# Optimization experiments

Hardware: AMD Instinct MI355X
Metric: run time of the kernel (lower is better)

Reference implementation:

```python
import jax, jax.numpy as jnp
import numpy as np

H, F, E, K = 1024, 4096, 8, 2
B, S = 2, 2048

def setup_inputs() -> dict:
    key = jax.random.key(0)
    ks = jax.random.split(key, 5)
    scale = 0.02
    return {
        "x": jax.random.normal(ks[0], (B, S, H), dtype=jnp.float32),
        "router_w": jax.random.normal(ks[1], (H, E), dtype=jnp.float32) * scale,
        "router_b": jnp.zeros((E,), dtype=jnp.float32),
        "w1": jax.random.normal(ks[2], (E, H, F), dtype=jnp.float32) * scale,
        "b1": jnp.zeros((E, F), dtype=jnp.float32),
        "w2": jax.random.normal(ks[3], (E, F, H), dtype=jnp.float32) * scale,
        "b2": jnp.zeros((E, H), dtype=jnp.float32),
        "k": K,
    }

def reference(x, router_w, router_b, w1, b1, w2, b2, k):
    # Router: softmax over experts, then top-k
    scores = jnp.einsum('bsh,he->bse', x, router_w) + router_b          # [B,S,E]
    probs = jax.nn.softmax(scores, axis=-1)
    p, expert_id = jax.lax.top_k(probs, k)                               # [B,S,k]
    # Dense all-expert MLP (math identical to per-expert gather/scatter)
    h = jax.nn.gelu(jnp.einsum('bsh,ehf->bsef', x, w1) + b1,
                    approximate=False)                                    # [B,S,E,F]
    out_all = jnp.einsum('bsef,efh->bseh', h, w2) + b2                    # [B,S,E,H]
    # Gather the k selected experts per token
    out = jnp.take_along_axis(out_all, expert_id[..., None], axis=2)     # [B,S,k,H]
    # Normalize top-k probs and combine
    p = p / jnp.sum(p, axis=-1, keepdims=True)                            # [B,S,k]
    return jnp.sum(p[..., None] * out, axis=2)                            # [B,S,H]
```

## Files before the change

### kernel.cpp

```cpp
#include <hip/hip_runtime.h>
#include <hip/hip_bf16.h>
#include <math.h>

#define H 1024
#define F 4096
#define E 8
#define NTOK 4096
#define CAP 4096
#define MCAP 2048
#define NPAIR 8192

typedef unsigned short u16;
typedef __bf16 bf16x8 __attribute__((ext_vector_type(8)));
typedef float f32x4 __attribute__((ext_vector_type(4)));
typedef u16 u16x8 __attribute__((ext_vector_type(8)));

__device__ inline u16 f2bf(float f) {
    union { float f; unsigned u; } v; v.f = f;
    unsigned r = v.u + 0x7fffu + ((v.u >> 16) & 1u);
    return (u16)(r >> 16);
}

__global__ void cvt_x(const float* __restrict__ x, u16* __restrict__ xb, int n4) {
    int j = blockIdx.x * blockDim.x + threadIdx.x;
    if (j >= n4) return;
    float4 v = ((const float4*)x)[j];
    u16x8 dummy; (void)dummy;
    u16* o = xb + (size_t)j * 4;
    o[0] = f2bf(v.x); o[1] = f2bf(v.y); o[2] = f2bf(v.z); o[3] = f2bf(v.w);
}

__global__ void transpose_cvt(const float* __restrict__ in, u16* __restrict__ out,
                              int R, int C) {
    const float* ip = in + (size_t)blockIdx.z * R * C;
    u16* op = out + (size_t)blockIdx.z * R * C;
    __shared__ float tile[32][33];
    int c0 = blockIdx.x * 32, r0 = blockIdx.y * 32;
    int tx = threadIdx.x, ty = threadIdx.y;
    for (int j = ty; j < 32; j += 8)
        tile[j][tx] = ip[(size_t)(r0 + j) * C + c0 + tx];
    __syncthreads();
    for (int j = ty; j < 32; j += 8)
        op[(size_t)(c0 + j) * R + r0 + tx] = f2bf(tile[tx][j]);
}

__global__ void router_kernel(const float* __restrict__ x, const float* __restrict__ rw,
                              const float* __restrict__ rb, int* __restrict__ counts,
                              int* __restrict__ tok_e, float* __restrict__ wgt_e) {
    int tok = blockIdx.x;
    int lane = threadIdx.x;
    float s[E] = {0.f,0.f,0.f,0.f,0.f,0.f,0.f,0.f};
    for (int r = 0; r < 4; ++r) {
        int h = r * 256 + lane * 4;
        float4 xv = *(const float4*)&x[(size_t)tok * H + h];
        const float* xf = (const float*)&xv;
        #pragma unroll
        for (int u = 0; u < 4; ++u) {
            float xs = xf[u];
            const float4* row = (const float4*)&rw[(size_t)(h + u) * E];
            float4 a = row[0], b = row[1];
            s[0] += xs * a.x; s[1] += xs * a.y; s[2] += xs * a.z; s[3] += xs * a.w;
            s[4] += xs * b.x; s[5] += xs * b.y; s[6] += xs * b.z; s[7] += xs * b.w;
        }
    }
    #pragma unroll
    for (int off = 32; off > 0; off >>= 1)
        #pragma unroll
        for (int e2 = 0; e2 < E; ++e2) s[e2] += __shfl_down(s[e2], off);
    if (lane == 0) {
        #pragma unroll
        for (int e2 = 0; e2 < E; ++e2) s[e2] += rb[e2];
        int i0 = 0;
        #pragma unroll
        for (int e2 = 1; e2 < E; ++e2) if (s[e2] > s[i0]) i0 = e2;
        int i1 = (i0 == 0) ? 1 : 0;
        #pragma unroll
        for (int e2 = 0; e2 < E; ++e2) if (e2 != i0 && s[e2] > s[i1]) i1 = e2;
        float p0 = 1.0f / (1.0f + expf(s[i1] - s[i0]));
        float p1 = 1.0f - p0;
        int pos0 = atomicAdd(&counts[i0], 1);
        tok_e[i0 * CAP + pos0] = tok; wgt_e[i0 * CAP + pos0] = p0;
        int pos1 = atomicAdd(&counts[i1], 1);
        tok_e[i1 * CAP + pos1] = tok; wgt_e[i1 * CAP + pos1] = p1;
    }
}

__global__ void scan_kernel(const int* __restrict__ counts, int* __restrict__ offsets) {
    if (threadIdx.x == 0 && blockIdx.x == 0) {
        int acc = 0;
        for (int e2 = 0; e2 < E; ++e2) { offsets[e2] = acc; acc += counts[e2]; }
    }
}

#define BM 128
#define BN 128
#define BK 32
#define LDP 40

__global__ void gemm1_kernel(const u16* __restrict__ xb, const u16* __restrict__ w1t,
                             const float* __restrict__ b1,
                             const int* __restrict__ counts, const int* __restrict__ offsets,
                             const int* __restrict__ tok_e, u16* __restrict__ hbuf) {
    int e = blockIdx.z;
    int rows = counts[e];
    int m0 = blockIdx.y * BM;
    if (m0 >= rows) return;
    int n0 = blockIdx.x * BN;
    int off = offsets[e];
    const u16* wB = w1t + (size_t)e * F * H;

    __shared__ u16 As[BM][LDP];
    __shared__ u16 Bs[BN][LDP];

    int tid = threadIdx.x;
    int lane = tid & 63;
    int w = tid >> 6;
    int wr = w >> 1, wc = w & 1;

    int ar0 = tid >> 2, ac0 = tid & 3;
    int ar1 = ar0 + 64;
    int ia0 = m0 + ar0; if (ia0 > rows - 1) ia0 = rows - 1;
    int ia1 = m0 + ar1; if (ia1 > rows - 1) ia1 = rows - 1;
    int t0 = tok_e[e * CAP + ia0];
    int t1 = tok_e[e * CAP + ia1];
    const u16* aR0 = xb + (size_t)t0 * H + ac0 * 8;
    const u16* aR1 = xb + (size_t)t1 * H + ac0 * 8;
    const u16* bR0 = wB + (size_t)(n0 + ar0) * H + ac0 * 8;
    const u16* bR1 = wB + (size_t)(n0 + ar1) * H + ac0 * 8;

    f32x4 acc[4][4] = {};

    for (int k0 = 0; k0 < H; k0 += BK) {
        u16x8 av0 = *(const u16x8*)(aR0 + k0);
        u16x8 av1 = *(const u16x8*)(aR1 + k0);
        u16x8 bv0 = *(const u16x8*)(bR0 + k0);
        u16x8 bv1 = *(const u16x8*)(bR1 + k0);
        __syncthreads();
        *(u16x8*)&As[ar0][ac0 * 8] = av0;
        *(u16x8*)&As[ar1][ac0 * 8] = av1;
        *(u16x8*)&Bs[ar0][ac0 * 8] = bv0;
        *(u16x8*)&Bs[ar1][ac0 * 8] = bv1;
        __syncthreads();
        bf16x8 af[4], bfr[4];
        int fr = lane & 15, fk = (lane >> 4) * 8;
        #pragma unroll
        for (int m = 0; m < 4; ++m) af[m] = *(bf16x8*)&As[wr * 64 + m * 16 + fr][fk];
        #pragma unroll
        for (int n = 0; n < 4; ++n) bfr[n] = *(bf16x8*)&Bs[wc * 64 + n * 16 + fr][fk];
        #pragma unroll
        for (int m = 0; m < 4; ++m)
            #pragma unroll
            for (int n = 0; n < 4; ++n)
                acc[m][n] = __builtin_amdgcn_mfma_f32_16x16x32_bf16(af[m], bfr[n], acc[m][n], 0, 0, 0);
    }

    const float* b1e = b1 + (size_t)e * F;
    int cr = (lane >> 4) * 4;
    int cc = lane & 15;
    #pragma unroll
    for (int m = 0; m < 4; ++m) {
        int gr = m0 + wr * 64 + m * 16 + cr;
        #pragma unroll
        for (int n = 0; n < 4; ++n) {
            int gc = n0 + wc * 64 + n * 16 + cc;
            float bias = b1e[gc];
            #pragma unroll
            for (int j = 0; j < 4; ++j) {
                int r = gr + j;
                if (r < rows) {
                    float v = acc[m][n][j] + bias;
                    float g = 0.5f * v * (1.0f + erff(v * 0.70710678118654752f));
                    hbuf[(size_t)(off + r) * F + gc] = f2bf(g);
                }
            }
        }
    }
}

__global__ void gemm2_kernel(const u16* __restrict__ hbuf, const u16* __restrict__ w2t,
                             const float* __restrict__ b2,
                             const int* __restrict__ counts, const int* __restrict__ offsets,
                             const int* __restrict__ tok_e, const float* __restrict__ wgt_e,
                             float* __restrict__ out) {
    int e = blockIdx.z;
    int rows = counts[e];
    int m0 = blockIdx.y * BM;
    if (m0 >= rows) return;
    int n0 = blockIdx.x * BN;
    int off = offsets[e];
    const u16* wB = w2t + (size_t)e * H * F;

    __shared__ u16 As[BM][LDP];
    __shared__ u16 Bs[BN][LDP];

    int tid = threadIdx.x;
    int lane = tid & 63;
    int w = tid >> 6;
    int wr = w >> 1, wc = w & 1;

    int ar0 = tid >> 2, ac0 = tid & 3;
    int ar1 = ar0 + 64;
    int ia0 = m0 + ar0; if (ia0 > rows - 1) ia0 = rows - 1;
    int ia1 = m0 + ar1; if (ia1 > rows - 1) ia1 = rows - 1;
    const u16* aR0 = hbuf + (size_t)(off + ia0) * F + ac0 * 8;
    const u16* aR1 = hbuf + (size_t)(off + ia1) * F + ac0 * 8;
    const u16* bR0 = wB + (size_t)(n0 + ar0) * F + ac0 * 8;
    const u16* bR1 = wB + (size_t)(n0 + ar1) * F + ac0 * 8;

    f32x4 acc[4][4] = {};

    for (int k0 = 0; k0 < F; k0 += BK) {
        u16x8 av0 = *(const u16x8*)(aR0 + k0);
        u16x8 av1 = *(const u16x8*)(aR1 + k0);
        u16x8 bv0 = *(const u16x8*)(bR0 + k0);
        u16x8 bv1 = *(const u16x8*)(bR1 + k0);
        __syncthreads();
        *(u16x8*)&As[ar0][ac0 * 8] = av0;
        *(u16x8*)&As[ar1][ac0 * 8] = av1;
        *(u16x8*)&Bs[ar0][ac0 * 8] = bv0;
        *(u16x8*)&Bs[ar1][ac0 * 8] = bv1;
        __syncthreads();
        bf16x8 af[4], bfr[4];
        int fr = lane & 15, fk = (lane >> 4) * 8;
        #pragma unroll
        for (int m = 0; m < 4; ++m) af[m] = *(bf16x8*)&As[wr * 64 + m * 16 + fr][fk];
        #pragma unroll
        for (int n = 0; n < 4; ++n) bfr[n] = *(bf16x8*)&Bs[wc * 64 + n * 16 + fr][fk];
        #pragma unroll
        for (int m = 0; m < 4; ++m)
            #pragma unroll
            for (int n = 0; n < 4; ++n)
                acc[m][n] = __builtin_amdgcn_mfma_f32_16x16x32_bf16(af[m], bfr[n], acc[m][n], 0, 0, 0);
    }

    const float* b2e = b2 + (size_t)e * H;
    int cr = (lane >> 4) * 4;
    int cc = lane & 15;
    #pragma unroll
    for (int m = 0; m < 4; ++m) {
        int gr = m0 + wr * 64 + m * 16 + cr;
        #pragma unroll
        for (int j = 0; j < 4; ++j) {
            int r = gr + j;
            if (r < rows) {
                int tok = tok_e[e * CAP + r];
                float wgt = wgt_e[e * CAP + r];
                #pragma unroll
                for (int n = 0; n < 4; ++n) {
                    int gc = n0 + wc * 64 + n * 16 + cc;
                    float v = (acc[m][n][j] + b2e[gc]) * wgt;
                    atomicAdd(&out[(size_t)tok * H + gc], v);
                }
            }
        }
    }
}

extern "C" void kernel_launch(void* const* d_in, const int* in_sizes, int n_in,
                              void* d_out, int out_size, void* d_ws, size_t ws_size,
                              hipStream_t stream) {
    const float* x  = (const float*)d_in[0];
    const float* rw = (const float*)d_in[1];
    const float* rb = (const float*)d_in[2];
    const float* w1 = (const float*)d_in[3];
    const float* b1 = (const float*)d_in[4];
    const float* w2 = (const float*)d_in[5];
    const float* b2 = (const float*)d_in[6];
    float* out = (float*)d_out;

    char* ws = (char*)d_ws;
    size_t o = 0;
    u16* xb   = (u16*)(ws + o); o += (size_t)NTOK * H * 2;
    u16* w1t  = (u16*)(ws + o); o += (size_t)E * F * H * 2;
    u16* w2t  = (u16*)(ws + o); o += (size_t)E * H * F * 2;
    u16* hbuf = (u16*)(ws + o); o += (size_t)NPAIR * F * 2;
    int*   tok_e = (int*)(ws + o);   o += (size_t)E * CAP * 4;
    float* wgt_e = (float*)(ws + o); o += (size_t)E * CAP * 4;
    int*   counts  = (int*)(ws + o); o += E * 4;
    int*   offsets = (int*)(ws + o); o += E * 4;

    hipMemsetAsync(counts, 0, 2 * E * sizeof(int), stream);
    hipMemsetAsync(out, 0, (size_t)out_size * sizeof(float), stream);

    cvt_x<<<(NTOK * H / 4 + 255) / 256, 256, 0, stream>>>(x, xb, NTOK * H / 4);
    transpose_cvt<<<dim3(F / 32, H / 32, E), dim3(32, 8), 0, stream>>>(w1, w1t, H, F);
    transpose_cvt<<<dim3(H / 32, F / 32, E), dim3(32, 8), 0, stream>>>(w2, w2t, F, H);
    router_kernel<<<NTOK, 64, 0, stream>>>(x, rw, rb, counts, tok_e, wgt_e);
    scan_kernel<<<1, 64, 0, stream>>>(counts, offsets);
    gemm1_kernel<<<dim3(F / BN, MCAP / BM, E), 256, 0, stream>>>(xb, w1t, b1, counts, offsets, tok_e, hbuf);
    gemm2_kernel<<<dim3(H / BN, MCAP / BM, E), 256, 0, stream>>>(hbuf, w2t, b2, counts, offsets, tok_e, wgt_e, out);
}
```

Before: 800.5 us.

## Use direct global-to-LDS loads in expert GEMMs and vectorize conversion kernels

The expert GEMMs now stage tiles with global_load_lds (buffer loads that write straight into LDS), dropping the register round trip and padded LDS layout. MFMA operands are swapped so each lane holds four consecutive columns, which allows vector bias loads and 8-byte bf16 stores in the GELU epilogue. The x-conversion and weight transpose kernels use wider vector loads and stores with 64x64 tiles. The grid M dimension grows from MCAP to CAP to cover experts with more than 2048 tokens, which fixes a correctness risk but launches more early-exit blocks. The unpadded LDS layout may cause bank conflicts on fragment reads.

Result: faster. 776.2 us (-3.0%).

```diff
diff --git a/kernel.cpp b/kernel.cpp
--- a/kernel.cpp
+++ b/kernel.cpp
@@ -7,13 +7,13 @@
 #define E 8
 #define NTOK 4096
 #define CAP 4096
-#define MCAP 2048
 #define NPAIR 8192
 
 typedef unsigned short u16;
 typedef __bf16 bf16x8 __attribute__((ext_vector_type(8)));
 typedef float f32x4 __attribute__((ext_vector_type(4)));
 typedef u16 u16x8 __attribute__((ext_vector_type(8)));
+typedef u16 u16x4 __attribute__((ext_vector_type(4)));
 
 __device__ inline u16 f2bf(float f) {
     union { float f; unsigned u; } v; v.f = f;
@@ -21,27 +21,50 @@
     return (u16)(r >> 16);
 }
 
-__global__ void cvt_x(const float* __restrict__ x, u16* __restrict__ xb, int n4) {
+__device__ inline void gload_lds16(const void* g, void* l) {
+    __builtin_amdgcn_global_load_lds(
+        (const __attribute__((address_space(1))) unsigned*)g,
+        (__attribute__((address_space(3))) unsigned*)l, 16, 0, 0);
+}
+
+__global__ void cvt_x(const float* __restrict__ x, u16* __restrict__ xb, int n8) {
     int j = blockIdx.x * blockDim.x + threadIdx.x;
-    if (j >= n4) return;
-    float4 v = ((const float4*)x)[j];
-    u16x8 dummy; (void)dummy;
-    u16* o = xb + (size_t)j * 4;
-    o[0] = f2bf(v.x); o[1] = f2bf(v.y); o[2] = f2bf(v.z); o[3] = f2bf(v.w);
+    if (j >= n8) return;
+    const float4* p = (const float4*)(x + (size_t)j * 8);
+    float4 a = p[0], b = p[1];
+    u16x8 o;
+    o[0] = f2bf(a.x); o[1] = f2bf(a.y); o[2] = f2bf(a.z); o[3] = f2bf(a.w);
+    o[4] = f2bf(b.x); o[5] = f2bf(b.y); o[6] = f2bf(b.z); o[7] = f2bf(b.w);
+    *(u16x8*)(xb + (size_t)j * 8) = o;
 }
 
 __global__ void transpose_cvt(const float* __restrict__ in, u16* __restrict__ out,
                               int R, int C) {
     const float* ip = in + (size_t)blockIdx.z * R * C;
     u16* op = out + (size_t)blockIdx.z * R * C;
-    __shared__ float tile[32][33];
-    int c0 = blockIdx.x * 32, r0 = blockIdx.y * 32;
-    int tx = threadIdx.x, ty = threadIdx.y;
-    for (int j = ty; j < 32; j += 8)
-        tile[j][tx] = ip[(size_t)(r0 + j) * C + c0 + tx];
+    __shared__ float tile[64][65];
+    int r0 = blockIdx.y * 64, c0 = blockIdx.x * 64;
+    int tid = threadIdx.x;
+    int rr = tid >> 4;
+    int cc4 = (tid & 15) * 4;
+    #pragma unroll
+    for (int it = 0; it < 4; ++it) {
+        int r = rr + it * 16;
+        float4 v = *(const float4*)&ip[(size_t)(r0 + r) * C + c0 + cc4];
+        tile[r][cc4 + 0] = v.x; tile[r][cc4 + 1] = v.y;
+        tile[r][cc4 + 2] = v.z; tile[r][cc4 + 3] = v.w;
+    }
     __syncthreads();
-    for (int j = ty; j < 32; j += 8)
-        op[(size_t)(c0 + j) * R + r0 + tx] = f2bf(tile[tx][j]);
+    int co = tid >> 3;
+    int ro8 = (tid & 7) * 8;
+    #pragma unroll
+    for (int it = 0; it < 2; ++it) {
+        int c = co + it * 32;
+        u16x8 o;
+        #pragma unroll
+        for (int u = 0; u < 8; ++u) o[u] = f2bf(tile[ro8 + u][c]);
+        *(u16x8*)&op[(size_t)(c0 + c) * R + r0 + ro8] = o;
+    }
 }
 
 __global__ void router_kernel(const float* __restrict__ x, const float* __restrict__ rw,
@@ -95,7 +118,6 @@
 #define BM 128
 #define BN 128
 #define BK 32
-#define LDP 40
 
 __global__ void gemm1_kernel(const u16* __restrict__ xb, const u16* __restrict__ w1t,
                              const float* __restrict__ b1,
@@ -109,69 +131,69 @@
     int off = offsets[e];
     const u16* wB = w1t + (size_t)e * F * H;
 
-    __shared__ u16 As[BM][LDP];
-    __shared__ u16 Bs[BN][LDP];
-
-    int tid = threadIdx.x;
-    int lane = tid & 63;
-    int w = tid >> 6;
+    __shared__ u16 As[BM * BK];
+    __shared__ u16 Bs[BN * BK];
+
+    int tid = threadIdx.x, lane = tid & 63, w = tid >> 6;
     int wr = w >> 1, wc = w & 1;
 
-    int ar0 = tid >> 2, ac0 = tid & 3;
-    int ar1 = ar0 + 64;
-    int ia0 = m0 + ar0; if (ia0 > rows - 1) ia0 = rows - 1;
-    int ia1 = m0 + ar1; if (ia1 > rows - 1) ia1 = rows - 1;
-    int t0 = tok_e[e * CAP + ia0];
-    int t1 = tok_e[e * CAP + ia1];
-    const u16* aR0 = xb + (size_t)t0 * H + ac0 * 8;
-    const u16* aR1 = xb + (size_t)t1 * H + ac0 * 8;
-    const u16* bR0 = wB + (size_t)(n0 + ar0) * H + ac0 * 8;
-    const u16* bR1 = wB + (size_t)(n0 + ar1) * H + ac0 * 8;
+    int i0 = w * 2, i1 = w * 2 + 1;
+    int rA0 = i0 * 16 + (lane >> 2), rA1 = i1 * 16 + (lane >> 2);
+    int cB = (lane & 3) * 8;
+    int ia0 = m0 + rA0; if (ia0 >= rows) ia0 = rows - 1;
+    int ia1 = m0 + rA1; if (ia1 >= rows) ia1 = rows - 1;
+    const u16* aS0 = xb + (size_t)tok_e[e * CAP + ia0] * H + cB;
+    const u16* aS1 = xb + (size_t)tok_e[e * CAP + ia1] * H + cB;
+    const u16* bS0 = wB + (size_t)(n0 + rA0) * H + cB;
+    const u16* bS1 = wB + (size_t)(n0 + rA1) * H + cB;
+    u16* lA0 = As + i0 * 512;  u16* lA1 = As + i1 * 512;
+    u16* lB0 = Bs + i0 * 512;  u16* lB1 = Bs + i1 * 512;
+
+    int fr = lane & 15, fk = (lane >> 4) * 8;
+    const u16* pa = As + (wr * 64 + fr) * BK + fk;
+    const u16* pb = Bs + (wc * 64 + fr) * BK + fk;
 
     f32x4 acc[4][4] = {};
 
     for (int k0 = 0; k0 < H; k0 += BK) {
-        u16x8 av0 = *(const u16x8*)(aR0 + k0);
-        u16x8 av1 = *(const u16x8*)(aR1 + k0);
-        u16x8 bv0 = *(const u16x8*)(bR0 + k0);
-        u16x8 bv1 = *(const u16x8*)(bR1 + k0);
         __syncthreads();
-        *(u16x8*)&As[ar0][ac0 * 8] = av0;
-        *(u16x8*)&As[ar1][ac0 * 8] = av1;
-        *(u16x8*)&Bs[ar0][ac0 * 8] = bv0;
-        *(u16x8*)&Bs[ar1][ac0 * 8] = bv1;
+        gload_lds16(aS0 + k0, lA0);
+        gload_lds16(aS1 + k0, lA1);
+        gload_lds16(bS0 + k0, lB0);
+        gload_lds16(bS1 + k0, lB1);
         __syncthreads();
         bf16x8 af[4], bfr[4];
-        int fr = lane & 15, fk = (lane >> 4) * 8;
-        #pragma unroll
-        for (int m = 0; m < 4; ++m) af[m] = *(bf16x8*)&As[wr * 64 + m * 16 + fr][fk];
-        #pragma unroll
-        for (int n = 0; n < 4; ++n) bfr[n] = *(bf16x8*)&Bs[wc * 64 + n * 16 + fr][fk];
+        #pragma unroll
+        for (int m = 0; m < 4; ++m) af[m] = *(const bf16x8*)(pa + m * 16 * BK);
+        #pragma unroll
+        for (int n = 0; n < 4; ++n) bfr[n] = *(const bf16x8*)(pb + n * 16 * BK);
         #pragma unroll
         for (int m = 0; m < 4; ++m)
             #pragma unroll
             for (int n = 0; n < 4; ++n)
-                acc[m][n] = __builtin_amdgcn_mfma_f32_16x16x32_bf16(af[m], bfr[n], acc[m][n], 0, 0, 0);
+                acc[m][n] = __builtin_amdgcn_mfma_f32_16x16x32_bf16(bfr[n], af[m], acc[m][n], 0, 0, 0);
     }
 
     const float* b1e = b1 + (size_t)e * F;
-    int cr = (lane >> 4) * 4;
-    int cc = lane & 15;
+    int c4 = (lane >> 4) * 4;
     #pragma unroll
     for (int m = 0; m < 4; ++m) {
-        int gr = m0 + wr * 64 + m * 16 + cr;
-        #pragma unroll
-        for (int n = 0; n < 4; ++n) {
-            int gc = n0 + wc * 64 + n * 16 + cc;
-            float bias = b1e[gc];
+        int r = m0 + wr * 64 + m * 16 + fr;
+        if (r < rows) {
+            u16* hrow = hbuf + (size_t)(off + r) * F;
             #pragma unroll
-            for (int j = 0; j < 4; ++j) {
-                int r = gr + j;
-                if (r < rows) {
-                    float v = acc[m][n][j] + bias;
+            for (int n = 0; n < 4; ++n) {
+                int gc = n0 + wc * 64 + n * 16 + c4;
+                float4 bv = *(const float4*)&b1e[gc];
+                const float* bvf = (const float*)&bv;
+                u16x4 ov;
+                #pragma unroll
+                for (int j = 0; j < 4; ++j) {
+                    float v = acc[m][n][j] + bvf[j];
                     float g = 0.5f * v * (1.0f + erff(v * 0.70710678118654752f));
-                    hbuf[(size_t)(off + r) * F + gc] = f2bf(g);
+                    ov[j] = f2bf(g);
                 }
+                *(u16x4*)&hrow[gc] = ov;
             }
         }
     }
@@ -190,67 +212,66 @@
     int off = offsets[e];
     const u16* wB = w2t + (size_t)e * H * F;
 
-    __shared__ u16 As[BM][LDP];
-    __shared__ u16 Bs[BN][LDP];
-
-    int tid = threadIdx.x;
-    int lane = tid & 63;
-    int w = tid >> 6;
+    __shared__ u16 As[BM * BK];
+    __shared__ u16 Bs[BN * BK];
+
+    int tid = threadIdx.x, lane = tid & 63, w = tid >> 6;
     int wr = w >> 1, wc = w & 1;
 
-    int ar0 = tid >> 2, ac0 = tid & 3;
-    int ar1 = ar0 + 64;
-    int ia0 = m0 + ar0; if (ia0 > rows - 1) ia0 = rows - 1;
-    int ia1 = m0 + ar1; if (ia1 > rows - 1) ia1 = rows - 1;
-    const u16* aR0 = hbuf + (size_t)(off + ia0) * F + ac0 * 8;
-    const u16* aR1 = hbuf + (size_t)(off + ia1) * F + ac0 * 8;
-    const u16* bR0 = wB + (size_t)(n0 + ar0) * F + ac0 * 8;
-    const u16* bR1 = wB + (size_t)(n0 + ar1) * F + ac0 * 8;
+    int i0 = w * 2, i1 = w * 2 + 1;
+    int rA0 = i0 * 16 + (lane >> 2), rA1 = i1 * 16 + (lane >> 2);
+    int cB = (lane & 3) * 8;
+    int ia0 = m0 + rA0; if (ia0 >= rows) ia0 = rows - 1;
+    int ia1 = m0 + rA1; if (ia1 >= rows) ia1 = rows - 1;
+    const u16* aS0 = hbuf + (size_t)(off + ia0) * F + cB;
+    const u16* aS1 = hbuf + (size_t)(off + ia1) * F + cB;
+    const u16* bS0 = wB + (size_t)(n0 + rA0) * F + cB;
+    const u16* bS1 = wB + (size_t)(n0 + rA1) * F + cB;
+    u16* lA0 = As + i0 * 512;  u16* lA1 = As + i1 * 512;
+    u16* lB0 = Bs + i0 * 512;  u16* lB1 = Bs + i1 * 512;
+
+    int fr = lane & 15, fk = (lane >> 4) * 8;
+    const u16* pa = As + (wr * 64 + fr) * BK + fk;
+    const u16* pb = Bs + (wc * 64 + fr) * BK + fk;
 
     f32x4 acc[4][4] = {};
 
     for (int k0 = 0; k0 < F; k0 += BK) {
-        u16x8 av0 = *(const u16x8*)(aR0 + k0);
-        u16x8 av1 = *(const u16x8*)(aR1 + k0);
-        u16x8 bv0 = *(const u16x8*)(bR0 + k0);
-        u16x8 bv1 = *(const u16x8*)(bR1 + k0);
         __syncthreads();
-        *(u16x8*)&As[ar0][ac0 * 8] = av0;
-        *(u16x8*)&As[ar1][ac0 * 8] = av1;
-        *(u16x8*)&Bs[ar0][ac0 * 8] = bv0;
-        *(u16x8*)&Bs[ar1][ac0 * 8] = bv1;
+        gload_lds16(aS0 + k0, lA0);
+        gload_lds16(aS1 + k0, lA1);
+        gload_lds16(bS0 + k0, lB0);
+        gload_lds16(bS1 + k0, lB1);
         __syncthreads();
         bf16x8 af[4], bfr[4];
-        int fr = lane & 15, fk = (lane >> 4) * 8;
-        #pragma unroll
-        for (int m = 0; m < 4; ++m) af[m] = *(bf16x8*)&As[wr * 64 + m * 16 + fr][fk];
-        #pragma unroll
-        for (int n = 0; n < 4; ++n) bfr[n] = *(bf16x8*)&Bs[wc * 64 + n * 16 + fr][fk];
+        #pragma unroll
+        for (int m = 0; m < 4; ++m) af[m] = *(const bf16x8*)(pa + m * 16 * BK);
+        #pragma unroll
+        for (int n = 0; n < 4; ++n) bfr[n] = *(const bf16x8*)(pb + n * 16 * BK);
         #pragma unroll
         for (int m = 0; m < 4; ++m)
             #pragma unroll
             for (int n = 0; n < 4; ++n)
-                acc[m][n] = __builtin_amdgcn_mfma_f32_16x16x32_bf16(af[m], bfr[n], acc[m][n], 0, 0, 0);
+                acc[m][n] = __builtin_amdgcn_mfma_f32_16x16x32_bf16(bfr[n], af[m], acc[m][n], 0, 0, 0);
     }
 
     const float* b2e = b2 + (size_t)e * H;
-    int cr = (lane >> 4) * 4;
-    int cc = lane & 15;
+    int c4 = (lane >> 4) * 4;
     #pragma unroll
     for (int m = 0; m < 4; ++m) {
-        int gr = m0 + wr * 64 + m * 16 + cr;
-        #pragma unroll
-        for (int j = 0; j < 4; ++j) {
-            int r = gr + j;
-            if (r < rows) {
-                int tok = tok_e[e * CAP + r];
-                float wgt = wgt_e[e * CAP + r];
+        int r = m0 + wr * 64 + m * 16 + fr;
+        if (r < rows) {
+            int tok = tok_e[e * CAP + r];
+            float wgt = wgt_e[e * CAP + r];
+            float* orow = out + (size_t)tok * H;
+            #pragma unroll
+            for (int n = 0; n < 4; ++n) {
+                int gc = n0 + wc * 64 + n * 16 + c4;
+                float4 bv = *(const float4*)&b2e[gc];
+                const float* bvf = (const float*)&bv;
                 #pragma unroll
-                for (int n = 0; n < 4; ++n) {
-                    int gc = n0 + wc * 64 + n * 16 + cc;
-                    float v = (acc[m][n][j] + b2e[gc]) * wgt;
-                    atomicAdd(&out[(size_t)tok * H + gc], v);
-                }
+                for (int j = 0; j < 4; ++j)
+                    atomicAdd(&orow[gc + j], (acc[m][n][j] + bvf[j]) * wgt);
             }
         }
     }
@@ -282,11 +303,11 @@
     hipMemsetAsync(counts, 0, 2 * E * sizeof(int), stream);
     hipMemsetAsync(out, 0, (size_t)out_size * sizeof(float), stream);
 
-    cvt_x<<<(NTOK * H / 4 + 255) / 256, 256, 0, stream>>>(x, xb, NTOK * H / 4);
-    transpose_cvt<<<dim3(F / 32, H / 32, E), dim3(32, 8), 0, stream>>>(w1, w1t, H, F);
-    transpose_cvt<<<dim3(H / 32, F / 32, E), dim3(32, 8), 0, stream>>>(w2, w2t, F, H);
+    cvt_x<<<(NTOK * H / 8 + 255) / 256, 256, 0, stream>>>(x, xb, NTOK * H / 8);
+    transpose_cvt<<<dim3(F / 64, H / 64, E), 256, 0, stream>>>(w1, w1t, H, F);
+    transpose_cvt<<<dim3(H / 64, F / 64, E), 256, 0, stream>>>(w2, w2t, F, H);
     router_kernel<<<NTOK, 64, 0, stream>>>(x, rw, rb, counts, tok_e, wgt_e);
     scan_kernel<<<1, 64, 0, stream>>>(counts, offsets);
-    gemm1_kernel<<<dim3(F / BN, MCAP / BM, E), 256, 0, stream>>>(xb, w1t, b1, counts, offsets, tok_e, hbuf);
-    gemm2_kernel<<<dim3(H / BN, MCAP / BM, E), 256, 0, stream>>>(hbuf, w2t, b2, counts, offsets, tok_e, wgt_e, out);
-}
+    gemm1_kernel<<<dim3(F / BN, CAP / BM, E), 256, 0, stream>>>(xb, w1t, b1, counts, offsets, tok_e, hbuf);
+    gemm2_kernel<<<dim3(H / BN, CAP / BM, E), 256, 0, stream>>>(hbuf, w2t, b2, counts, offsets, tok_e, wgt_e, out);
+}
```
